# Optimization experiments

Hardware: AMD Instinct MI355X
Metric: run time of the kernel (lower is better)

## Reference

```python
import jax, jax.numpy as jnp
import numpy as np

BN_EPS = 1e-5
NORM_EPS = 1e-12  # F.normalize default eps


def reference(x, conv_w, bn_gamma, bn_beta):
    # 1x1 conv dimension reduction: [B,2048,H,W] -> [B,256,H,W]
    z = jnp.einsum('bchw,dc->bdhw', x, conv_w)
    # BatchNorm2d (training-mode batch statistics) + ReLU
    mu = z.mean(axis=(0, 2, 3), keepdims=True)
    var = z.var(axis=(0, 2, 3), keepdims=True)
    z = (z - mu) / jnp.sqrt(var + BN_EPS)
    z = z * bn_gamma.reshape(1, -1, 1, 1) + bn_beta.reshape(1, -1, 1, 1)
    z = jax.nn.relu(z)

    B, d, h, w = z.shape
    M = h * w
    xm = z.reshape(B, d, M)
    # Covpool: y = x I_hat x^T with I_hat = (I - 11^T/M)/M == centered 2nd moment
    xc = xm - xm.mean(axis=-1, keepdims=True)
    cov = jnp.einsum('bdm,bem->bde', xc, xc) / M  # [B,d,d]

    # Eigen decomposition (cov is symmetric PSD; SVD of PSD == eigh)
    s, U = jnp.linalg.eigh(cov)  # s: [B,d], U: [B,d,d]
    eps = jnp.finfo(cov.dtype).eps
    s = jnp.maximum(s, eps)

    # ExponentialInverse: U exp(-S) U^T
    inv_x = jnp.einsum('bid,bd,bjd->bij', U, jnp.exp(-s), U)
    # Power (matrix sqrt): U S^{1/2} U^T
    out = jnp.einsum('bid,bd,bjd->bij', U, jnp.sqrt(s), U)

    # attention = out @ inv_x^T  (inv_x is symmetric, transpose kept for fidelity)
    att = jnp.einsum('bij,bkj->bik', out, inv_x)
    flat = att.reshape(B, -1)
    nrm = jnp.maximum(jnp.linalg.norm(flat, axis=1, keepdims=True), NORM_EPS)
    normalized = (flat / nrm).reshape(att.shape)
    att = out * (att / normalized)

    y = att + out
    iu = jnp.triu_indices(d)
    return y[:, iu[0], iu[1]]  # [B, d*(d+1)/2]


def setup_inputs() -> dict:
    key = jax.random.key(0)
    k1, k2 = jax.random.split(key)
    x = jax.random.normal(k1, (32, 2048, 28, 28), dtype=jnp.float32)
    # kaiming-normal fan_out scaling for 1x1 conv: std = sqrt(2/fan_out)=sqrt(2/256)
    conv_w = jax.random.normal(k2, (256, 2048), dtype=jnp.float32) * np.sqrt(2.0 / 256.0)
    bn_gamma = jnp.ones((256,), dtype=jnp.float32)
    bn_beta = jnp.zeros((256,), dtype=jnp.float32)
    return {'x': x, 'conv_w': conv_w, 'bn_gamma': bn_gamma, 'bn_beta': bn_beta}
```

## Files before the change

### kernel.cpp

```cpp
#include <hip/hip_runtime.h>


typedef unsigned short u16;
typedef __attribute__((ext_vector_type(8))) short bf16x8;
typedef __attribute__((ext_vector_type(4))) float f32x4;

__device__ __forceinline__ u16 f2bf(float f) {
  unsigned u = __builtin_bit_cast(unsigned, f);
  u += 0x7FFFu + ((u >> 16) & 1u);
  return (u16)(u >> 16);
}
__device__ __forceinline__ float bf2f(u16 h) {
  unsigned u = ((unsigned)h) << 16;
  return __builtin_bit_cast(float, u);
}

__device__ __forceinline__
void mm_core(const u16* __restrict__ Ah, const u16* __restrict__ Al,
             const u16* __restrict__ Bh, const u16* __restrict__ Bl,
             long boff, int row0, int col0,
             u16 (*lds)[128][8][8], f32x4 acc[4][4])
{
  const int tid = threadIdx.x;
  const int wave = tid >> 6, lane = tid & 63;
  const int wm = wave >> 1, wn = wave & 1;
  const int mL = lane & 15, q = lane >> 4;
  const u16* baseA[2] = {Ah + boff, Al + boff};
  const u16* baseB[2] = {Bh + boff, Bl + boff};

  for (int k0 = 0; k0 < 256; k0 += 64) {
    __syncthreads();
#pragma unroll
    for (int it = 0; it < 16; ++it) {
      const int t = it >> 2;
      const int r = ((it & 3) << 8) + tid;
      const int m = r >> 3, c = r & 7;
      const u16* src = (t < 2 ? baseA[t] : baseB[t - 2])
                     + (long)((t < 2 ? row0 : col0) + m) * 256 + k0 + c * 8;
      const uint4 v = *reinterpret_cast<const uint4*>(src);
      *reinterpret_cast<uint4*>(&lds[t][m][c ^ (m & 7)][0]) = v;
    }
    __syncthreads();
#pragma unroll
    for (int kk = 0; kk < 2; ++kk) {
      bf16x8 ah[4], al[4], bh[4], bl[4];
#pragma unroll
      for (int i = 0; i < 4; ++i) {
        const int ma = wm * 64 + i * 16 + mL;
        const int ca = (kk * 4 + q) ^ (ma & 7);
        ah[i] = *reinterpret_cast<const bf16x8*>(&lds[0][ma][ca][0]);
        al[i] = *reinterpret_cast<const bf16x8*>(&lds[1][ma][ca][0]);
        const int nb = wn * 64 + i * 16 + mL;
        const int cb = (kk * 4 + q) ^ (nb & 7);
        bh[i] = *reinterpret_cast<const bf16x8*>(&lds[2][nb][cb][0]);
        bl[i] = *reinterpret_cast<const bf16x8*>(&lds[3][nb][cb][0]);
      }
#pragma unroll
      for (int i = 0; i < 4; ++i)
#pragma unroll
        for (int j = 0; j < 4; ++j) {
          acc[i][j] = __builtin_amdgcn_mfma_f32_16x16x32_bf16(ah[i], bh[j], acc[i][j], 0, 0, 0);
          acc[i][j] = __builtin_amdgcn_mfma_f32_16x16x32_bf16(ah[i], bl[j], acc[i][j], 0, 0, 0);
          acc[i][j] = __builtin_amdgcn_mfma_f32_16x16x32_bf16(al[i], bh[j], acc[i][j], 0, 0, 0);
        }
    }
  }
}

template<int MB>
__global__ __launch_bounds__(256)
void fuse_k(const u16* __restrict__ A0, const u16* __restrict__ B0, u16* __restrict__ C0,
            float al0, float b10, float dg0, const float* __restrict__ cf0,
            const u16* __restrict__ A1, const u16* __restrict__ B1, u16* __restrict__ C1,
            u16* __restrict__ D1, float al1, float b11, float dg1,
            float hc1, float hc2, float hc3, const float* __restrict__ cf1, long LO)
{
  __shared__ u16 lds[4][128][8][8];
  int z = blockIdx.z;
  const bool hB = (z >= 32);
  const u16 *Ah, *Bh; u16 *C, *D = nullptr;
  float al, b1, dg; const float* cf;
  if (!hB) { Ah = A0; Bh = B0; C = C0; al = al0; b1 = b10; dg = dg0; cf = cf0; }
  else { z -= 32; Ah = A1; Bh = B1; C = C1; D = D1; al = al1; b1 = b11; dg = dg1; cf = cf1; }
  const long boff = (long)z * 65536;
  const int row0 = blockIdx.y * 128, col0 = blockIdx.x * 128;
  const int wave = threadIdx.x >> 6, lane = threadIdx.x & 63;
  const int wm = wave >> 1, wn = wave & 1;
  const int mL = lane & 15, q = lane >> 4;

  f32x4 acc[4][4];
#pragma unroll
  for (int i = 0; i < 4; ++i)
#pragma unroll
    for (int j = 0; j < 4; ++j) acc[i][j] = {0.f, 0.f, 0.f, 0.f};

  mm_core(Ah, Ah + LO, Bh, Bh + LO, boff, row0, col0, lds, acc);

#pragma unroll
  for (int i = 0; i < 4; ++i) {
    const int rbase = row0 + wm * 64 + i * 16 + q * 4;
#pragma unroll
    for (int j = 0; j < 4; ++j) {
      const int cc = col0 + wn * 64 + j * 16 + mL;
#pragma unroll
      for (int rg = 0; rg < 4; ++rg) {
        const int rr = rbase + rg;
        const long o = boff + (long)rr * 256 + cc;
        const float vr = acc[i][j][rg];
        if (MB == 1 && hB) {
          u16 h = f2bf(vr);
          C[o] = h; C[o + LO] = f2bf(vr - bf2f(h));
          float hv = fmaf(vr, hc1, cf[o] * hc2);
          if (rr == cc) hv += hc3;
          h = f2bf(hv);
          D[o] = h; D[o + LO] = f2bf(hv - bf2f(h));
        } else {
          float v = al * vr;
          if (cf) v = fmaf(b1, cf[o], v);
          if (rr == cc) v += dg;
          const u16 h = f2bf(v);
          C[o] = h; C[o + LO] = f2bf(v - bf2f(h));
        }
      }
    }
  }
}

__global__ __launch_bounds__(256)
void gemm2_pair_k(const u16* __restrict__ A0, const u16* __restrict__ B0, u16* __restrict__ C0,
                  const u16* __restrict__ A1, const u16* __restrict__ B1, u16* __restrict__ C1,
                  long LO)
{
  __shared__ u16 lds[4][128][8][8];
  int z = blockIdx.z;
  const u16 *Ah, *Bh; u16* Chp;
  if (z < 32) { Ah = A0; Bh = B0; Chp = C0; }
  else { z -= 32; Ah = A1; Bh = B1; Chp = C1; }
  const long boff = (long)z * 65536;
  const int row0 = blockIdx.y * 128, col0 = blockIdx.x * 128;
  const int wave = threadIdx.x >> 6, lane = threadIdx.x & 63;
  const int wm = wave >> 1, wn = wave & 1;
  const int mL = lane & 15, q = lane >> 4;

  f32x4 acc[4][4];
#pragma unroll
  for (int i = 0; i < 4; ++i)
#pragma unroll
    for (int j = 0; j < 4; ++j) acc[i][j] = {0.f, 0.f, 0.f, 0.f};

  mm_core(Ah, Ah + LO, Bh, Bh + LO, boff, row0, col0, lds, acc);

#pragma unroll
  for (int i = 0; i < 4; ++i) {
    const int rbase = row0 + wm * 64 + i * 16 + q * 4;
#pragma unroll
    for (int j = 0; j < 4; ++j) {
      const int cc = col0 + wn * 64 + j * 16 + mL;
#pragma unroll
      for (int rg = 0; rg < 4; ++rg) {
        const long o = boff + (long)(rbase + rg) * 256 + cc;
        const float v = acc[i][j][rg];
        const u16 h = f2bf(v);
        Chp[o] = h; Chp[o + LO] = f2bf(v - bf2f(h));
      }
    }
  }
}

template<int MODE>
__global__ __launch_bounds__(256)
void gemmN64_k(const u16* __restrict__ Ah, const u16* __restrict__ Al,
               const u16* __restrict__ Bh, const u16* __restrict__ Bl,
               u16* __restrict__ Ch, u16* __restrict__ Cl,
               const float* __restrict__ cf, float alpha, float b1, float diag,
               float* __restrict__ attn2)
{
  __shared__ u16 ldsA[2][128][8][8];
  __shared__ u16 ldsB[2][64][8][8];
  const long boff = (long)blockIdx.z * 65536;
  const int row0 = blockIdx.y * 128, col0 = blockIdx.x * 64;
  const int tid = threadIdx.x;
  const int wave = tid >> 6, lane = tid & 63;
  const int wm = wave >> 1, wn = wave & 1;
  const int mL = lane & 15, q = lane >> 4;
  const u16* baseA[2] = {Ah + boff, Al + boff};
  const u16* baseB[2] = {Bh + boff, Bl + boff};

  f32x4 acc[4][2];
#pragma unroll
  for (int i = 0; i < 4; ++i)
#pragma unroll
    for (int j = 0; j < 2; ++j) acc[i][j] = {0.f, 0.f, 0.f, 0.f};

  for (int k0 = 0; k0 < 256; k0 += 64) {
    __syncthreads();
#pragma unroll
    for (int it = 0; it < 8; ++it) {
      const int t = it >> 2;
      const int r = ((it & 3) << 8) + tid;
      const int m = r >> 3, c = r & 7;
      const uint4 v = *reinterpret_cast<const uint4*>(
          baseA[t] + (long)(row0 + m) * 256 + k0 + c * 8);
      *reinterpret_cast<uint4*>(&ldsA[t][m][c ^ (m & 7)][0]) = v;
    }
#pragma unroll
    for (int it = 0; it < 4; ++it) {
      const int t = it >> 1;
      const int r = ((it & 1) << 8) + tid;
      const int m = r >> 3, c = r & 7;
      const uint4 v = *reinterpret_cast<const uint4*>(
          baseB[t] + (long)(col0 + m) * 256 + k0 + c * 8);
      *reinterpret_cast<uint4*>(&ldsB[t][m][c ^ (m & 7)][0]) = v;
    }
    __syncthreads();
#pragma unroll
    for (int kk = 0; kk < 2; ++kk) {
      bf16x8 ah[4], alo[4], bh[2], bl[2];
#pragma unroll
      for (int i = 0; i < 4; ++i) {
        const int ma = wm * 64 + i * 16 + mL;
        const int ca = (kk * 4 + q) ^ (ma & 7);
        ah[i]  = *reinterpret_cast<const bf16x8*>(&ldsA[0][ma][ca][0]);
        alo[i] = *reinterpret_cast<const bf16x8*>(&ldsA[1][ma][ca][0]);
      }
#pragma unroll
      for (int j = 0; j < 2; ++j) {
        const int nb = wn * 32 + j * 16 + mL;
        const int cb = (kk * 4 + q) ^ (nb & 7);
        bh[j] = *reinterpret_cast<const bf16x8*>(&ldsB[0][nb][cb][0]);
        bl[j] = *reinterpret_cast<const bf16x8*>(&ldsB[1][nb][cb][0]);
      }
#pragma unroll
      for (int i = 0; i < 4; ++i)
#pragma unroll
        for (int j = 0; j < 2; ++j) {
          acc[i][j] = __builtin_amdgcn_mfma_f32_16x16x32_bf16(ah[i],  bh[j], acc[i][j], 0, 0, 0);
          acc[i][j] = __builtin_amdgcn_mfma_f32_16x16x32_bf16(ah[i],  bl[j], acc[i][j], 0, 0, 0);
          acc[i][j] = __builtin_amdgcn_mfma_f32_16x16x32_bf16(alo[i], bh[j], acc[i][j], 0, 0, 0);
        }
    }
  }

  if (MODE == 2) {
    float ssum = 0.f;
#pragma unroll
    for (int i = 0; i < 4; ++i)
#pragma unroll
      for (int j = 0; j < 2; ++j)
#pragma unroll
        for (int rg = 0; rg < 4; ++rg) ssum = fmaf(acc[i][j][rg], acc[i][j][rg], ssum);
#pragma unroll
    for (int o = 32; o > 0; o >>= 1) ssum += __shfl_down(ssum, o);
    __syncthreads();
    float* red = (float*)&ldsA[0][0][0][0];
    if (lane == 0) red[wave] = ssum;
    __syncthreads();
    if (tid == 0)
      atomicAdd(attn2 + blockIdx.z, red[0] + red[1] + red[2] + red[3]);
    return;
  }

#pragma unroll
  for (int i = 0; i < 4; ++i) {
    const int rbase = row0 + wm * 64 + i * 16 + q * 4;
#pragma unroll
    for (int j = 0; j < 2; ++j) {
      const int cc = col0 + wn * 32 + j * 16 + mL;
#pragma unroll
      for (int rg = 0; rg < 4; ++rg) {
        const int rr = rbase + rg;
        const long o = boff + (long)rr * 256 + cc;
        float v = alpha * acc[i][j][rg];
        if (cf) v = fmaf(b1, cf[o], v);
        if (rr == cc) v += diag;
        const u16 h = f2bf(v);
        Ch[o] = h; Cl[o] = f2bf(v - bf2f(h));
      }
    }
  }
}

__global__ __launch_bounds__(512)
void conv_k(const float* __restrict__ w, const float* __restrict__ x,
            float* __restrict__ z)
{
  __shared__ u16 ldsA[256][8][8];
  __shared__ u16 ldsB[128][8][8];
  const int tid = threadIdx.x;
  const int b = blockIdx.z;
  const int n0 = blockIdx.x * 128;
  const int wave = tid >> 6, lane = tid & 63;
  const int wm = wave >> 1, wn = wave & 1;
  const int mL = lane & 15, q = lane >> 4;
  const float* xb = x + (long)b * 2048 * 784;

  f32x4 acc[4][4];
#pragma unroll
  for (int i = 0; i < 4; ++i)
#pragma unroll
    for (int j = 0; j < 4; ++j) acc[i][j] = {0.f, 0.f, 0.f, 0.f};

  for (int k0 = 0; k0 < 2048; k0 += 64) {
    __syncthreads();
#pragma unroll
    for (int it = 0; it < 4; ++it) {
      const int g = it * 512 + tid;
      const int m = g >> 3, c = g & 7;
      const float4 f0 = *reinterpret_cast<const float4*>(w + (long)m * 2048 + k0 + c * 8);
      const float4 f1 = *reinterpret_cast<const float4*>(w + (long)m * 2048 + k0 + c * 8 + 4);
      ushort4 ua, ub;
      ua.x = f2bf(f0.x); ua.y = f2bf(f0.y); ua.z = f2bf(f0.z); ua.w = f2bf(f0.w);
      ub.x = f2bf(f1.x); ub.y = f2bf(f1.y); ub.z = f2bf(f1.z); ub.w = f2bf(f1.w);
      *reinterpret_cast<ushort4*>(&ldsA[m][c ^ (m & 7)][0]) = ua;
      *reinterpret_cast<ushort4*>(&ldsA[m][c ^ (m & 7)][4]) = ub;
    }
    {
      const int kg = tid >> 5, nc = tid & 31;
      const int kbase = kg * 4, nbase = nc * 4;
      float vv[4][4];
#pragma unroll
      for (int jk = 0; jk < 4; ++jk) {
        const int gk = k0 + kbase + jk;
        const int gn = n0 + nbase;
        float4 f = make_float4(0.f, 0.f, 0.f, 0.f);
        if (gn < 784) f = *reinterpret_cast<const float4*>(xb + (long)gk * 784 + gn);
        vv[jk][0] = f.x; vv[jk][1] = f.y; vv[jk][2] = f.z; vv[jk][3] = f.w;
      }
      const int c = kbase >> 3, ko = kbase & 7;
#pragma unroll
      for (int jn = 0; jn < 4; ++jn) {
        const int n = nbase + jn;
        ushort4 u;
        u.x = f2bf(vv[0][jn]); u.y = f2bf(vv[1][jn]);
        u.z = f2bf(vv[2][jn]); u.w = f2bf(vv[3][jn]);
        *reinterpret_cast<ushort4*>(&ldsB[n][c ^ (n & 7)][ko]) = u;
      }
    }
    __syncthreads();
#pragma unroll
    for (int kk = 0; kk < 2; ++kk) {
      bf16x8 af[4], bfv[4];
#pragma unroll
      for (int i = 0; i < 4; ++i) {
        const int ma = wm * 64 + i * 16 + mL;
        af[i] = *reinterpret_cast<const bf16x8*>(&ldsA[ma][(kk * 4 + q) ^ (ma & 7)][0]);
        const int nb = wn * 64 + i * 16 + mL;
        bfv[i] = *reinterpret_cast<const bf16x8*>(&ldsB[nb][(kk * 4 + q) ^ (nb & 7)][0]);
      }
#pragma unroll
      for (int i = 0; i < 4; ++i)
#pragma unroll
        for (int j = 0; j < 4; ++j)
          acc[i][j] = __builtin_amdgcn_mfma_f32_16x16x32_bf16(af[i], bfv[j], acc[i][j], 0, 0, 0);
    }
  }
#pragma unroll
  for (int i = 0; i < 4; ++i) {
    const int rbase = wm * 64 + i * 16 + q * 4;
#pragma unroll
    for (int j = 0; j < 4; ++j) {
      const int cc = n0 + wn * 64 + j * 16 + mL;
      if (cc >= 784) continue;
#pragma unroll
      for (int rg = 0; rg < 4; ++rg)
        z[((long)b * 256 + rbase + rg) * 784 + cc] = acc[i][j][rg];
    }
  }
}

__global__ __launch_bounds__(256)
void gram_k(const u16* __restrict__ zb, const float* __restrict__ rs,
            float* __restrict__ cov, u16* __restrict__ C2h, u16* __restrict__ C2l)
{
  __shared__ u16 lds[2][128][8][8];
  const int tid = threadIdx.x;
  const int b = blockIdx.z;
  const int col0 = blockIdx.x * 128, row0 = blockIdx.y * 128;
  const int wave = tid >> 6, lane = tid & 63;
  const int wm = wave >> 1, wn = wave & 1;
  const int mL = lane & 15, q = lane >> 4;
  const u16* zbb = zb + (long)b * 256 * 832;

  f32x4 acc[4][4];
#pragma unroll
  for (int i = 0; i < 4; ++i)
#pragma unroll
    for (int j = 0; j < 4; ++j) acc[i][j] = {0.f, 0.f, 0.f, 0.f};

  for (int k0 = 0; k0 < 832; k0 += 64) {
    __syncthreads();
#pragma unroll
    for (int it = 0; it < 8; ++it) {
      const int t = it >> 2;
      const int r = ((it & 3) << 8) + tid;
      const int m = r >> 3, c = r & 7;
      const int grow = (t == 0 ? row0 : col0) + m;
      const uint4 v = *reinterpret_cast<const uint4*>(zbb + (long)grow * 832 + k0 + c * 8);
      *reinterpret_cast<uint4*>(&lds[t][m][c ^ (m & 7)][0]) = v;
    }
    __syncthreads();
#pragma unroll
    for (int kk = 0; kk < 2; ++kk) {
      bf16x8 af[4], bfv[4];
#pragma unroll
      for (int i = 0; i < 4; ++i) {
        const int ma = wm * 64 + i * 16 + mL;
        af[i] = *reinterpret_cast<const bf16x8*>(&lds[0][ma][(kk * 4 + q) ^ (ma & 7)][0]);
        const int nb = wn * 64 + i * 16 + mL;
        bfv[i] = *reinterpret_cast<const bf16x8*>(&lds[1][nb][(kk * 4 + q) ^ (nb & 7)][0]);
      }
#pragma unroll
      for (int i = 0; i < 4; ++i)
#pragma unroll
        for (int j = 0; j < 4; ++j)
          acc[i][j] = __builtin_amdgcn_mfma_f32_16x16x32_bf16(af[i], bfv[j], acc[i][j], 0, 0, 0);
    }
  }
  const float inv_m = 1.f / 784.f;
#pragma unroll
  for (int i = 0; i < 4; ++i) {
    const int rr0 = row0 + wm * 64 + i * 16 + q * 4;
#pragma unroll
    for (int j = 0; j < 4; ++j) {
      const int cc = col0 + wn * 64 + j * 16 + mL;
      const float mu_c = rs[b * 256 + cc] * inv_m;
#pragma unroll
      for (int rg = 0; rg < 4; ++rg) {
        const int rr = rr0 + rg;
        const float mu_r = rs[b * 256 + rr] * inv_m;
        const long o = ((long)b * 256 + rr) * 256 + cc;
        const float cv = fmaf(acc[i][j][rg], inv_m, -mu_r * mu_c);
        cov[o] = cv;
        const u16 h = f2bf(cv);
        C2h[o] = h; C2l[o] = f2bf(cv - bf2f(h));
      }
    }
  }
}

__global__ __launch_bounds__(256)
void bn_stats_k(const float* __restrict__ z, float* __restrict__ ps,
                float* __restrict__ pq)
{
  const int d = blockIdx.x, sl = blockIdx.y, t = threadIdx.x;
  const int lane = t & 63, wid = t >> 6;
  __shared__ float ws[4], wq[4];
  float s = 0.f, qq = 0.f;
  for (int b = sl * 4; b < sl * 4 + 4; ++b) {
    const float* p = z + ((long)b * 256 + d) * 784;
    for (int m = t; m < 784; m += 256) {
      const float v = p[m];
      s += v; qq = fmaf(v, v, qq);
    }
  }
#pragma unroll
  for (int o = 32; o > 0; o >>= 1) { s += __shfl_down(s, o); qq += __shfl_down(qq, o); }
  if (lane == 0) { ws[wid] = s; wq[wid] = qq; }
  __syncthreads();
  if (t == 0) {
    ps[d * 8 + sl] = ws[0] + ws[1] + ws[2] + ws[3];
    pq[d * 8 + sl] = wq[0] + wq[1] + wq[2] + wq[3];
  }
}

__global__ __launch_bounds__(256)
void bn_apply_k(const float* __restrict__ z, const float* __restrict__ gamma,
                const float* __restrict__ beta, const float* __restrict__ ps,
                const float* __restrict__ pq, u16* __restrict__ zb,
                float* __restrict__ rs)
{
  const int d = blockIdx.x, b = blockIdx.y, t = threadIdx.x;
  const int lane = t & 63, wid = t >> 6;
  __shared__ float bc[2], ws[4];
  if (t == 0) {
    float sum = 0.f, sq = 0.f;
#pragma unroll
    for (int s8 = 0; s8 < 8; ++s8) { sum += ps[d * 8 + s8]; sq += pq[d * 8 + s8]; }
    const float inv_n = 1.f / 25088.f;
    const float mean = sum * inv_n;
    const float var = sq * inv_n - mean * mean;
    const float sc = gamma[d] * rsqrtf(var + 1e-5f);
    bc[0] = sc; bc[1] = fmaf(-mean, sc, beta[d]);
  }
  __syncthreads();
  const float sc = bc[0], sh = bc[1];
  const float* p = z + ((long)b * 256 + d) * 784;
  u16* qp = zb + ((long)b * 256 + d) * 832;
  float rsum = 0.f;
  for (int m = t; m < 832; m += 256) {
    const float v = (m < 784) ? fmaxf(fmaf(p[m], sc, sh), 0.f) : 0.f;
    qp[m] = f2bf(v);
    rsum += v;
  }
#pragma unroll
  for (int o = 32; o > 0; o >>= 1) rsum += __shfl_down(rsum, o);
  if (lane == 0) ws[wid] = rsum;
  __syncthreads();
  if (t == 0) rs[b * 256 + d] = ws[0] + ws[1] + ws[2] + ws[3];
}

__global__ __launch_bounds__(256)
void power_k(const float* __restrict__ cov, float* __restrict__ s,
             float* __restrict__ attn2)
{
  const int b = blockIdx.x, i = threadIdx.x;
  const float* A = cov + (long)b * 65536;
  __shared__ float v[256];
  __shared__ float red[4];
  v[i] = 1.f;
  __syncthreads();
  float lam = 1.f;
  for (int it = 0; it < 10; ++it) {
    float u = 0.f;
#pragma unroll 8
    for (int j = 0; j < 256; ++j) u = fmaf(A[(long)j * 256 + i], v[j], u);
    float ss = u * u;
#pragma unroll
    for (int o = 32; o > 0; o >>= 1) ss += __shfl_down(ss, o);
    if ((i & 63) == 0) red[i >> 6] = ss;
    __syncthreads();
    lam = sqrtf(red[0] + red[1] + red[2] + red[3]);
    v[i] = u / lam;
    __syncthreads();
  }
  if (i == 0) { s[b] = 1.8f / lam; attn2[b] = 0.f; }
}

__global__ __launch_bounds__(256)
void init_k(const float* __restrict__ cov, const float* __restrict__ s,
            u16* __restrict__ Yh, u16* __restrict__ Yl,
            u16* __restrict__ Th, u16* __restrict__ Tl)
{
  const int b = blockIdx.y, i = blockIdx.x, j = threadIdx.x;
  const long o = ((long)b * 256 + i) * 256 + j;
  const float a = cov[o] * s[b];
  u16 h = f2bf(a);
  Yh[o] = h; Yl[o] = f2bf(a - bf2f(h));
  float tv = -0.5f * a;
  if (i == j) tv += 1.5f;
  h = f2bf(tv);
  Th[o] = h; Tl[o] = f2bf(tv - bf2f(h));
}

__global__ __launch_bounds__(256)
void out_k(const u16* __restrict__ Yh, const u16* __restrict__ Yl,
           const float* __restrict__ s, const float* __restrict__ attn2,
           float* __restrict__ out)
{
  const int i = blockIdx.x, b = blockIdx.y, j = threadIdx.x;
  if (j < i) return;
  const float inv = rsqrtf(s[b]);
  const float nrm = fmaxf(sqrtf(fmaxf(attn2[b], 0.f)) * inv, 1e-12f);
  const float scv = inv * (1.f + nrm);
  const long o = ((long)b * 256 + i) * 256 + j;
  const long off = (long)b * 32896 + (long)i * 256 - (long)i * (i - 1) / 2 + (j - i);
  out[off] = (bf2f(Yh[o]) + bf2f(Yl[o])) * scv;
}

extern "C" void kernel_launch(void* const* d_in, const int* in_sizes, int n_in,
                              void* d_out, int out_size, void* d_ws, size_t ws_size,
                              hipStream_t stream)
{
  const float* x     = (const float*)d_in[0];
  const float* w     = (const float*)d_in[1];
  const float* gamma = (const float*)d_in[2];
  const float* beta  = (const float*)d_in[3];
  float* out = (float*)d_out;

  const long PS = 4194304;
  const long LO = 2097152;
  u16* S[9];
  for (int k = 0; k < 9; ++k) S[k] = (u16*)d_ws + (long)k * PS;
  char* base = (char*)d_ws;
  float* z   = (float*)(base + 75497472);
  u16*   zb  = (u16*)(base + 101187584);
  float* cov = (float*)(base + 114819072);
  float* st  = (float*)(base + 123207680);
  float* sv = st, *attn2 = st + 32, *rs = st + 64;
  float* ps = st + 64 + 8192, *pq = ps + 2048;
  u16 *C2 = S[5], *V = S[6], *Ha = S[7], *Hb = S[8];

  const dim3 blk(256);
  const dim3 gP(2, 2, 64);
  const dim3 gT(4, 2, 32);
  const dim3 gE(256, 32);

  conv_k<<<dim3(7, 1, 32), dim3(512), 0, stream>>>(w, x, z);
  bn_stats_k<<<dim3(256, 8), blk, 0, stream>>>(z, ps, pq);
  bn_apply_k<<<dim3(256, 32), blk, 0, stream>>>(z, gamma, beta, ps, pq, zb, rs);
  gram_k<<<dim3(2, 2, 32), blk, 0, stream>>>(zb, rs, cov, C2, C2 + LO);
  power_k<<<dim3(32), blk, 0, stream>>>(cov, sv, attn2);
  init_k<<<gE, blk, 0, stream>>>(cov, sv, S[0], S[0] + LO, S[1], S[1] + LO);

  fuse_k<1><<<gP, blk, 0, stream>>>(
      S[0], S[1], S[2], 1.f, 0.f, 0.f, (const float*)nullptr,
      C2, C2, V, Ha, 1.f, 0.f, 0.f,
      1.f / 40320.f, -1.f / 5040.f, 1.f / 720.f, cov, LO);

  int iY = 2, iZ = 1, fa = 0, fb = 3, fc = 4;
  for (int it = 1; it <= 7; ++it) {
    const int iT = fa;
    if (it == 1)
      fuse_k<0><<<gP, blk, 0, stream>>>(
          S[iZ], S[iY], S[iT], -0.5f, 0.f, 1.5f, (const float*)nullptr,
          V, Ha, Hb, (u16*)nullptr, 1.f, -1.f / 120.f, 1.f / 24.f,
          0.f, 0.f, 0.f, cov, LO);
    else if (it == 2)
      fuse_k<0><<<gP, blk, 0, stream>>>(
          S[iZ], S[iY], S[iT], -0.5f, 0.f, 1.5f, (const float*)nullptr,
          V, Hb, Ha, (u16*)nullptr, 1.f, -1.f / 6.f, 0.5f,
          0.f, 0.f, 0.f, cov, LO);
    else if (it == 3)
      fuse_k<0><<<gP, blk, 0, stream>>>(
          S[iZ], S[iY], S[iT], -0.5f, 0.f, 1.5f, (const float*)nullptr,
          V, Ha, Hb, (u16*)nullptr, 1.f, -1.f, 1.f,
          0.f, 0.f, 0.f, cov, LO);
    else
      gemmN64_k<0><<<gT, blk, 0, stream>>>(
          S[iZ], S[iZ] + LO, S[iY], S[iY] + LO, S[iT], S[iT] + LO,
          (const float*)nullptr, -0.5f, 0.f, 1.5f, (float*)nullptr);
    if (it < 7) {
      gemm2_pair_k<<<gP, blk, 0, stream>>>(S[iY], S[iT], S[fb],
                                           S[iT], S[iZ], S[fc], LO);
      const int nY = fb, nZ = fc;
      fa = iY; fb = iZ; fc = iT;
      iY = nY; iZ = nZ;
    } else {
      gemmN64_k<0><<<gT, blk, 0, stream>>>(
          S[iY], S[iY] + LO, S[iT], S[iT] + LO, S[fb], S[fb] + LO,
          (const float*)nullptr, 1.f, 0.f, 0.f, (float*)nullptr);
      iY = fb;
    }
  }

  gemmN64_k<2><<<gT, blk, 0, stream>>>(
      S[iY], S[iY] + LO, Hb, Hb + LO, (u16*)nullptr, (u16*)nullptr,
      (const float*)nullptr, 1.f, 0.f, 0.f, attn2);
  out_k<<<gE, blk, 0, stream>>>(S[iY], S[iY] + LO, sv, attn2, out);
}
```

Measured before the change: 776.2 us.

## Pre-cast conv weights to bf16, split conv over M, widen power iteration

Adds a kernel that casts the conv weights to bf16 once into workspace (aliased with the cov buffer, which is written later). The conv kernel now reads the bf16 weights directly and is split across two 128-row output tiles with 256-thread blocks, doubling the grid from 224 to 448 blocks. The power iteration now uses 1024 threads, splitting the 256-long dot product into four partial sums combined through shared memory. The conv split means each block loads the x tile twice overall, doubling that global traffic, in exchange for more parallelism and no per-block weight conversion.

```diff
diff --git a/kernel.cpp b/kernel.cpp
--- a/kernel.cpp
+++ b/kernel.cpp
@@ -280,15 +280,16 @@
   }
 }
 
-__global__ __launch_bounds__(512)
-void conv_k(const float* __restrict__ w, const float* __restrict__ x,
+__global__ __launch_bounds__(256)
+void conv_k(const u16* __restrict__ wb, const float* __restrict__ x,
             float* __restrict__ z)
 {
-  __shared__ u16 ldsA[256][8][8];
+  __shared__ u16 ldsA[128][8][8];
   __shared__ u16 ldsB[128][8][8];
   const int tid = threadIdx.x;
   const int b = blockIdx.z;
   const int n0 = blockIdx.x * 128;
+  const int m0 = blockIdx.y * 128;
   const int wave = tid >> 6, lane = tid & 63;
   const int wm = wave >> 1, wn = wave & 1;
   const int mL = lane & 15, q = lane >> 4;
@@ -304,36 +305,36 @@
     __syncthreads();
 #pragma unroll
     for (int it = 0; it < 4; ++it) {
-      const int g = it * 512 + tid;
+      const int g = it * 256 + tid;
       const int m = g >> 3, c = g & 7;
-      const float4 f0 = *reinterpret_cast<const float4*>(w + (long)m * 2048 + k0 + c * 8);
-      const float4 f1 = *reinterpret_cast<const float4*>(w + (long)m * 2048 + k0 + c * 8 + 4);
-      ushort4 ua, ub;
-      ua.x = f2bf(f0.x); ua.y = f2bf(f0.y); ua.z = f2bf(f0.z); ua.w = f2bf(f0.w);
-      ub.x = f2bf(f1.x); ub.y = f2bf(f1.y); ub.z = f2bf(f1.z); ub.w = f2bf(f1.w);
-      *reinterpret_cast<ushort4*>(&ldsA[m][c ^ (m & 7)][0]) = ua;
-      *reinterpret_cast<ushort4*>(&ldsA[m][c ^ (m & 7)][4]) = ub;
+      const uint4 v = *reinterpret_cast<const uint4*>(
+          wb + (long)(m0 + m) * 2048 + k0 + c * 8);
+      *reinterpret_cast<uint4*>(&ldsA[m][c ^ (m & 7)][0]) = v;
     }
     {
       const int kg = tid >> 5, nc = tid & 31;
-      const int kbase = kg * 4, nbase = nc * 4;
-      float vv[4][4];
-#pragma unroll
-      for (int jk = 0; jk < 4; ++jk) {
-        const int gk = k0 + kbase + jk;
-        const int gn = n0 + nbase;
-        float4 f = make_float4(0.f, 0.f, 0.f, 0.f);
-        if (gn < 784) f = *reinterpret_cast<const float4*>(xb + (long)gk * 784 + gn);
-        vv[jk][0] = f.x; vv[jk][1] = f.y; vv[jk][2] = f.z; vv[jk][3] = f.w;
-      }
-      const int c = kbase >> 3, ko = kbase & 7;
-#pragma unroll
-      for (int jn = 0; jn < 4; ++jn) {
-        const int n = nbase + jn;
-        ushort4 u;
-        u.x = f2bf(vv[0][jn]); u.y = f2bf(vv[1][jn]);
-        u.z = f2bf(vv[2][jn]); u.w = f2bf(vv[3][jn]);
-        *reinterpret_cast<ushort4*>(&ldsB[n][c ^ (n & 7)][ko]) = u;
+      const int nbase = nc * 4;
+      const int gn = n0 + nbase;
+#pragma unroll
+      for (int half = 0; half < 2; ++half) {
+        const int kbase = kg * 4 + half * 32;
+        float vv[4][4];
+#pragma unroll
+        for (int jk = 0; jk < 4; ++jk) {
+          const int gk = k0 + kbase + jk;
+          float4 f = make_float4(0.f, 0.f, 0.f, 0.f);
+          if (gn < 784) f = *reinterpret_cast<const float4*>(xb + (long)gk * 784 + gn);
+          vv[jk][0] = f.x; vv[jk][1] = f.y; vv[jk][2] = f.z; vv[jk][3] = f.w;
+        }
+        const int c = kbase >> 3, ko = kbase & 7;
+#pragma unroll
+        for (int jn = 0; jn < 4; ++jn) {
+          const int n = nbase + jn;
+          ushort4 u;
+          u.x = f2bf(vv[0][jn]); u.y = f2bf(vv[1][jn]);
+          u.z = f2bf(vv[2][jn]); u.w = f2bf(vv[3][jn]);
+          *reinterpret_cast<ushort4*>(&ldsB[n][c ^ (n & 7)][ko]) = u;
+        }
       }
     }
     __syncthreads();
@@ -356,7 +357,7 @@
   }
 #pragma unroll
   for (int i = 0; i < 4; ++i) {
-    const int rbase = wm * 64 + i * 16 + q * 4;
+    const int rbase = m0 + wm * 64 + i * 16 + q * 4;
 #pragma unroll
     for (int j = 0; j < 4; ++j) {
       const int cc = n0 + wn * 64 + j * 16 + mL;
@@ -499,31 +500,39 @@
   if (t == 0) rs[b * 256 + d] = ws[0] + ws[1] + ws[2] + ws[3];
 }
 
-__global__ __launch_bounds__(256)
+__global__ __launch_bounds__(1024)
 void power_k(const float* __restrict__ cov, float* __restrict__ s,
              float* __restrict__ attn2)
 {
-  const int b = blockIdx.x, i = threadIdx.x;
+  const int b = blockIdx.x, tid = threadIdx.x;
+  const int i = tid & 255, g = tid >> 8;
   const float* A = cov + (long)b * 65536;
   __shared__ float v[256];
+  __shared__ float part[4][256];
   __shared__ float red[4];
-  v[i] = 1.f;
+  if (g == 0) v[i] = 1.f;
   __syncthreads();
   float lam = 1.f;
   for (int it = 0; it < 10; ++it) {
     float u = 0.f;
+    const int jb = g * 64;
 #pragma unroll 8
-    for (int j = 0; j < 256; ++j) u = fmaf(A[(long)j * 256 + i], v[j], u);
-    float ss = u * u;
-#pragma unroll
-    for (int o = 32; o > 0; o >>= 1) ss += __shfl_down(ss, o);
-    if ((i & 63) == 0) red[i >> 6] = ss;
+    for (int j = jb; j < jb + 64; ++j) u = fmaf(A[(long)j * 256 + i], v[j], u);
+    part[g][i] = u;
+    __syncthreads();
+    if (g == 0) {
+      u = part[0][i] + part[1][i] + part[2][i] + part[3][i];
+      float ss = u * u;
+#pragma unroll
+      for (int o = 32; o > 0; o >>= 1) ss += __shfl_down(ss, o);
+      if ((i & 63) == 0) red[i >> 6] = ss;
+    }
     __syncthreads();
     lam = sqrtf(red[0] + red[1] + red[2] + red[3]);
-    v[i] = u / lam;
-    __syncthreads();
-  }
-  if (i == 0) { s[b] = 1.8f / lam; attn2[b] = 0.f; }
+    if (g == 0) v[i] = u / lam;
+    __syncthreads();
+  }
+  if (tid == 0) { s[b] = 1.8f / lam; attn2[b] = 0.f; }
 }
 
 __global__ __launch_bounds__(256)
@@ -557,6 +566,13 @@
   out[off] = (bf2f(Yh[o]) + bf2f(Yl[o])) * scv;
 }
 
+__global__ __launch_bounds__(256)
+void cast_w_k(const float* __restrict__ w, u16* __restrict__ wb)
+{
+  const int idx = blockIdx.x * 256 + threadIdx.x;
+  wb[idx] = f2bf(w[idx]);
+}
+
 extern "C" void kernel_launch(void* const* d_in, const int* in_sizes, int n_in,
                               void* d_out, int out_size, void* d_ws, size_t ws_size,
                               hipStream_t stream)
@@ -575,6 +591,7 @@
   float* z   = (float*)(base + 75497472);
   u16*   zb  = (u16*)(base + 101187584);
   float* cov = (float*)(base + 114819072);
+  u16*   wbuf = (u16*)(base + 114819072);
   float* st  = (float*)(base + 123207680);
   float* sv = st, *attn2 = st + 32, *rs = st + 64;
   float* ps = st + 64 + 8192, *pq = ps + 2048;
@@ -585,11 +602,12 @@
   const dim3 gT(4, 2, 32);
   const dim3 gE(256, 32);
 
-  conv_k<<<dim3(7, 1, 32), dim3(512), 0, stream>>>(w, x, z);
+  cast_w_k<<<dim3(2048), blk, 0, stream>>>(w, wbuf);
+  conv_k<<<dim3(7, 2, 32), blk, 0, stream>>>(wbuf, x, z);
   bn_stats_k<<<dim3(256, 8), blk, 0, stream>>>(z, ps, pq);
   bn_apply_k<<<dim3(256, 32), blk, 0, stream>>>(z, gamma, beta, ps, pq, zb, rs);
   gram_k<<<dim3(2, 2, 32), blk, 0, stream>>>(zb, rs, cov, C2, C2 + LO);
-  power_k<<<dim3(32), blk, 0, stream>>>(cov, sv, attn2);
+  power_k<<<dim3(32), dim3(1024), 0, stream>>>(cov, sv, attn2);
   init_k<<<gE, blk, 0, stream>>>(cov, sv, S[0], S[0] + LO, S[1], S[1] + LO);
 
   fuse_k<1><<<gP, blk, 0, stream>>>(
```

New measurement: 739.0 us. 1.05x faster.
